# Performance work log

Measured on AMD Instinct MI355X. Metric: run time of the kernel, lower is better.

## Reference

```python
import jax, jax.numpy as jnp
import numpy as np

D_MODEL, N_HEADS = 768, 12
D_K = D_MODEL // N_HEADS
NEG = -1e9


def setup_inputs() -> dict:
    key = jax.random.key(0)
    ks = jax.random.split(key, 12)
    B, S, D = 2, 4096, D_MODEL
    s = 1.0 / np.sqrt(D)
    inp = {
        'query': jax.random.normal(ks[0], (B, S, D), jnp.float32),
        'key': jax.random.normal(ks[1], (B, S, D), jnp.float32),
        'value': jax.random.normal(ks[2], (B, S, D), jnp.float32),
        'mask': jnp.ones((B, S), jnp.int32),
        'Wq': jax.random.normal(ks[3], (D, D), jnp.float32) * s,
        'bq': jnp.zeros((D,), jnp.float32),
        'Wk': jax.random.normal(ks[4], (D, D), jnp.float32) * s,
        'bk': jnp.zeros((D,), jnp.float32),
        'Wv': jax.random.normal(ks[5], (D, D), jnp.float32) * s,
        'bv': jnp.zeros((D,), jnp.float32),
        'Wo': jax.random.normal(ks[6], (D, D), jnp.float32) * s,
        'bo': jnp.zeros((D,), jnp.float32),
    }
    return inp


def reference(query, key, value, mask, Wq, bq, Wk, bk, Wv, bv, Wo, bo):
    B, Sq, D = query.shape
    Sk = key.shape[1]
    # torch Linear: x @ W.T + b; weights stored [out, in]
    def proj(x, W, b, S):
        return (x @ W.T + b).reshape(B, S, N_HEADS, D_K).transpose(0, 2, 1, 3)
    Q = proj(query, Wq, bq, Sq)   # [B,H,Sq,Dk]
    K = proj(key, Wk, bk, Sk)
    V = proj(value, Wv, bv, Sk)
    scores = jnp.einsum('bhqd,bhkd->bhqk', Q, K) / jnp.sqrt(jnp.float32(D_K))
    # padding mask on keys: [B,1,1,Sk]
    scores = jnp.where(mask[:, None, None, :] == 0, NEG, scores)
    # causal mask (triu, diagonal=1)
    causal = jnp.triu(jnp.ones((Sq, Sk), bool), k=1)
    scores = jnp.where(causal[None, None], NEG, scores)
    attn = jax.nn.softmax(scores, axis=-1)
    out = jnp.einsum('bhqk,bhkd->bhqd', attn, V)
    out = out.transpose(0, 2, 1, 3).reshape(B, Sq, D)
    return out @ Wo.T + bo
```

## Files before the change

kernel.cpp:

```cpp
#include <hip/hip_runtime.h>
#include <hip/hip_bf16.h>

#define D_MODEL 768
#define N_HEADS 12
#define D_K     64
#define NEG_INF (-1e9f)
#define SCALE_Q 0.1803368801111154f
#define W_ELEMS (D_MODEL * D_MODEL)

typedef __attribute__((ext_vector_type(8))) short          bf16x8;
typedef __attribute__((ext_vector_type(4))) float          floatx4;
typedef __attribute__((ext_vector_type(4))) unsigned short ushortx4;
typedef __attribute__((ext_vector_type(2))) unsigned int   uintx2;
typedef __attribute__((ext_vector_type(4))) unsigned int   uintx4;

static __device__ __forceinline__ unsigned short f2bf(float f) {
    unsigned u = __builtin_bit_cast(unsigned, f);
    u += 0x7FFFu + ((u >> 16) & 1u);
    return (unsigned short)(u >> 16);
}

static __device__ __forceinline__ float exp2_hw(float x) {
#if __has_builtin(__builtin_amdgcn_exp2f)
    return __builtin_amdgcn_exp2f(x);
#else
    return __builtin_exp2f(x);
#endif
}

static __device__ __forceinline__ float rcp_hw(float x) {
#if __has_builtin(__builtin_amdgcn_rcpf)
    return __builtin_amdgcn_rcpf(x);
#else
    return 1.f / x;
#endif
}

static __device__ __forceinline__ void gload_lds16(const void* g, void* l) {
    __builtin_amdgcn_global_load_lds(
        (const __attribute__((address_space(1))) void*)g,
        (__attribute__((address_space(3))) void*)l, 16, 0, 0);
}

__global__ __launch_bounds__(256) void convert_w4(
    const float* __restrict__ W0, const float* __restrict__ W1,
    const float* __restrict__ W2, const float* __restrict__ W3,
    unsigned short* __restrict__ out)
{
    const float* src[4] = {W0, W1, W2, W3};
    const float* W = src[blockIdx.y];
    unsigned short* o = out + (size_t)blockIdx.y * W_ELEMS;
    const int i = (blockIdx.x * 256 + threadIdx.x) * 4;
    float4 v = *(const float4*)(W + i);
    ushortx4 h = { f2bf(v.x), f2bf(v.y), f2bf(v.z), f2bf(v.w) };
    *(ushortx4*)(o + i) = h;
}

__global__ __launch_bounds__(256) void convert_a3(
    const float* __restrict__ A0, const float* __restrict__ A1,
    const float* __restrict__ A2,
    unsigned short* __restrict__ O0, unsigned short* __restrict__ O1,
    unsigned short* __restrict__ O2)
{
    const int z = blockIdx.y;
    const float* A = (z == 0) ? A0 : (z == 1) ? A1 : A2;
    unsigned short* O = (z == 0) ? O0 : (z == 1) ? O1 : O2;
    const int i = (blockIdx.x * 256 + threadIdx.x) * 4;
    float4 v = *(const float4*)(A + i);
    ushortx4 h = { f2bf(v.x), f2bf(v.y), f2bf(v.z), f2bf(v.w) };
    *(ushortx4*)(O + i) = h;
}

__global__ __launch_bounds__(256) void gemm128(
    const unsigned short* __restrict__ A0, const unsigned short* __restrict__ A1,
    const unsigned short* __restrict__ A2,
    const unsigned short* __restrict__ W0, const unsigned short* __restrict__ W1,
    const unsigned short* __restrict__ W2,
    const float* __restrict__ b0, const float* __restrict__ b1,
    const float* __restrict__ b2,
    void* __restrict__ C0, void* __restrict__ C1, void* __restrict__ C2,
    int S)
{
    __shared__ __align__(16) unsigned short As[128 * 32];
    __shared__ __align__(16) unsigned short Bs[128 * 32];

    const int z = blockIdx.z;
    const unsigned short* A = (z == 0) ? A0 : (z == 1) ? A1 : A2;
    const unsigned short* W = (z == 0) ? W0 : (z == 1) ? W1 : W2;
    const float* bias       = (z == 0) ? b0 : (z == 1) ? b1 : b2;
    void* C                 = (z == 0) ? C0 : (z == 1) ? C1 : C2;
    const float scale = (z == 0) ? SCALE_Q : 1.0f;
    const int mode = (z == 2) ? 3 : 1;

    const int tid  = threadIdx.x;
    const int wave = tid >> 6;
    const int lane = tid & 63;
    const int quad = lane >> 4;
    const int l16  = lane & 15;
    const int m0 = blockIdx.x * 128;
    const int n0 = blockIdx.y * 128;
    const int wm = (wave & 1) * 64;
    const int wn = (wave >> 1) * 64;
    const int sr = lane >> 2;
    const int sc = (lane & 3) << 3;

    const floatx4 zero4 = {0.f, 0.f, 0.f, 0.f};
    floatx4 acc[4][4];
    #pragma unroll
    for (int i = 0; i < 4; ++i)
        #pragma unroll
        for (int j = 0; j < 4; ++j) acc[i][j] = zero4;

    for (int k0 = 0; k0 < D_MODEL; k0 += 32) {
        #pragma unroll
        for (int c = 0; c < 2; ++c) {
            const int row = wave * 32 + c * 16;
            gload_lds16(A + (size_t)(m0 + row + sr) * D_MODEL + k0 + sc,
                        As + row * 32);
            gload_lds16(W + (size_t)(n0 + row + sr) * D_MODEL + k0 + sc,
                        Bs + row * 32);
        }
        __syncthreads();

        bf16x8 af[4], bfr[4];
        #pragma unroll
        for (int i = 0; i < 4; ++i)
            af[i] = *(const bf16x8*)(As + (wm + i * 16 + l16) * 32 + quad * 8);
        #pragma unroll
        for (int j = 0; j < 4; ++j)
            bfr[j] = *(const bf16x8*)(Bs + (wn + j * 16 + l16) * 32 + quad * 8);
        #pragma unroll
        for (int i = 0; i < 4; ++i)
            #pragma unroll
            for (int j = 0; j < 4; ++j)
                acc[i][j] = __builtin_amdgcn_mfma_f32_16x16x32_bf16(
                    bfr[j], af[i], acc[i][j], 0, 0, 0);
        __syncthreads();
    }

    #pragma unroll
    for (int i = 0; i < 4; ++i) {
        const int m = m0 + wm + i * 16 + l16;
        #pragma unroll
        for (int j = 0; j < 4; ++j) {
            const int nb = n0 + wn + j * 16 + quad * 4;
            const float4 bv = *(const float4*)(bias + nb);
            float v0 = (acc[i][j][0] + bv.x) * scale;
            float v1 = (acc[i][j][1] + bv.y) * scale;
            float v2 = (acc[i][j][2] + bv.z) * scale;
            float v3 = (acc[i][j][3] + bv.w) * scale;
            if (mode == 1) {
                ushortx4 o = {f2bf(v0), f2bf(v1), f2bf(v2), f2bf(v3)};
                *(ushortx4*)((unsigned short*)C + (size_t)m * D_MODEL + nb) = o;
            } else {
                const int bb = m / S, s = m - bb * S;
                const int hh = nb >> 6, d = nb & 63;
                unsigned short* base = (unsigned short*)C +
                    ((size_t)(bb * N_HEADS + hh) * D_K + d) * S + s;
                base[0]         = f2bf(v0);
                base[(size_t)S]     = f2bf(v1);
                base[(size_t)S * 2] = f2bf(v2);
                base[(size_t)S * 3] = f2bf(v3);
            }
        }
    }
}

__global__ __launch_bounds__(256) void gemm64o(
    const unsigned short* __restrict__ A,
    const unsigned short* __restrict__ W,
    const float* __restrict__ bias,
    float* __restrict__ C)
{
    __shared__ __align__(16) unsigned short As[64 * 32];
    __shared__ __align__(16) unsigned short Bs[128 * 32];

    const int tid  = threadIdx.x;
    const int wave = tid >> 6;
    const int lane = tid & 63;
    const int quad = lane >> 4;
    const int l16  = lane & 15;
    const int m0 = blockIdx.x * 64;
    const int n0 = blockIdx.y * 128;
    const int wn = wave * 32;
    const int sr = lane >> 2;
    const int sc = (lane & 3) << 3;

    const floatx4 zero4 = {0.f, 0.f, 0.f, 0.f};
    floatx4 acc[4][2];
    #pragma unroll
    for (int i = 0; i < 4; ++i)
        #pragma unroll
        for (int j = 0; j < 2; ++j) acc[i][j] = zero4;

    for (int k0 = 0; k0 < D_MODEL; k0 += 32) {
        if (wave < 2) {
            const int g0 = wave * 32;
            gload_lds16(A + (size_t)(m0 + g0 + sr) * D_MODEL + k0 + sc,
                        As + g0 * 32);
            gload_lds16(A + (size_t)(m0 + g0 + 16 + sr) * D_MODEL + k0 + sc,
                        As + (g0 + 16) * 32);
            const int bg = 96 + wave * 16;
            gload_lds16(W + (size_t)(n0 + bg + sr) * D_MODEL + k0 + sc,
                        Bs + bg * 32);
        } else {
            const int bg = (wave - 2) * 48;
            #pragma unroll
            for (int c = 0; c < 3; ++c)
                gload_lds16(W + (size_t)(n0 + bg + c * 16 + sr) * D_MODEL + k0 + sc,
                            Bs + (bg + c * 16) * 32);
        }
        __syncthreads();

        bf16x8 af[4], bfr[2];
        #pragma unroll
        for (int i = 0; i < 4; ++i)
            af[i] = *(const bf16x8*)(As + (i * 16 + l16) * 32 + quad * 8);
        #pragma unroll
        for (int j = 0; j < 2; ++j)
            bfr[j] = *(const bf16x8*)(Bs + (wn + j * 16 + l16) * 32 + quad * 8);
        #pragma unroll
        for (int i = 0; i < 4; ++i)
            #pragma unroll
            for (int j = 0; j < 2; ++j)
                acc[i][j] = __builtin_amdgcn_mfma_f32_16x16x32_bf16(
                    bfr[j], af[i], acc[i][j], 0, 0, 0);
        __syncthreads();
    }

    #pragma unroll
    for (int i = 0; i < 4; ++i) {
        const int m = m0 + i * 16 + l16;
        #pragma unroll
        for (int j = 0; j < 2; ++j) {
            const int nb = n0 + wn + j * 16 + quad * 4;
            const float4 bv = *(const float4*)(bias + nb);
            float4 o = {acc[i][j][0] + bv.x, acc[i][j][1] + bv.y,
                        acc[i][j][2] + bv.z, acc[i][j][3] + bv.w};
            *(float4*)(C + (size_t)m * D_MODEL + nb) = o;
        }
    }
}

__global__ __launch_bounds__(256) void flash_attn(
    const unsigned short* __restrict__ Qp,
    const unsigned short* __restrict__ Kp,
    const unsigned short* __restrict__ VpT,
    const int* __restrict__ mask,
    unsigned short* __restrict__ O,
    int S)
{
    __shared__ __align__(16) unsigned short Ks [2][64 * 64];
    __shared__ __align__(16) unsigned short Vts[2][64 * 64];
    __shared__ __align__(16) float mskf[2][64];

    const int L  = blockIdx.x;
    const int bh = L % 24;
    const int p  = L / 24;
    const int h  = bh % 12;
    const int b  = bh / 12;
    const int nqt = S >> 6;
    const int tid  = threadIdx.x;
    const int wave = tid >> 6;
    const int lane = tid & 63;
    const int quad = lane >> 4;
    const int l16  = lane & 15;
    const int sx   = (l16 & 7) << 3;
    const int qh   = wave & 1;
    const int kh2  = wave >> 1;

    const unsigned short* Kbase = Kp  + (size_t)(b * S) * D_MODEL + h * D_K;
    const unsigned short* Vbase = VpT + (size_t)(b * N_HEADS + h) * D_K * S;
    const int* mbase = mask + b * S;

    const int srow = wave * 8 + (lane >> 3);
    const int sgc  = ((lane & 7) ^ (lane >> 3)) << 3;

    const floatx4 zero4 = {0.f, 0.f, 0.f, 0.f};
    const short one_bf = (short)0x3F80;
    const bf16x8 ones = {one_bf, one_bf, one_bf, one_bf,
                         one_bf, one_bf, one_bf, one_bf};

    #pragma unroll
    for (int sel = 0; sel < 2; ++sel) {
        const int qt = sel ? (nqt - 1 - p) : p;
        const int q0 = qt * 64;

        bf16x8 qf[2][2];
        #pragma unroll
        for (int qg = 0; qg < 2; ++qg) {
            const size_t rowQ =
                (size_t)(b * S + q0 + qh * 32 + qg * 16 + l16) * D_MODEL + h * D_K;
            qf[qg][0] = *(const bf16x8*)(Qp + rowQ + quad * 8);
            qf[qg][1] = *(const bf16x8*)(Qp + rowQ + 32 + quad * 8);
        }

        floatx4 acc2[2][4];
        floatx4 accl[2];
        #pragma unroll
        for (int qg = 0; qg < 2; ++qg) {
            accl[qg] = zero4;
            #pragma unroll
            for (int dt = 0; dt < 4; ++dt) acc2[qg][dt] = zero4;
        }

        const int ni = qt + 1;

        #pragma unroll
        for (int c = 0; c < 2; ++c) {
            gload_lds16(Kbase + (size_t)(c * 32 + srow) * D_MODEL + sgc,
                        (char*)Ks[0] + (c * 4 + wave) * 1024);
            gload_lds16(Vbase + (size_t)(c * 32 + srow) * S + sgc,
                        (char*)Vts[0] + (c * 4 + wave) * 1024);
        }
        if (tid < 64) mskf[0][tid] = (mbase[tid] == 0) ? NEG_INF : 0.f;
        __syncthreads();

        for (int kt = 0; kt < ni; ++kt) {
            const int k0 = kt * 64;
            const int cur = kt & 1;

            if (kt + 1 < ni) {
                const int kn = k0 + 64;
                #pragma unroll
                for (int c = 0; c < 2; ++c) {
                    gload_lds16(
                        Kbase + (size_t)(kn + c * 32 + srow) * D_MODEL + sgc,
                        (char*)Ks[cur ^ 1] + (c * 4 + wave) * 1024);
                    gload_lds16(
                        Vbase + (size_t)(c * 32 + srow) * S + kn + sgc,
                        (char*)Vts[cur ^ 1] + (c * 4 + wave) * 1024);
                }
                if (tid < 64)
                    mskf[cur ^ 1][tid] = (mbase[kn + tid] == 0) ? NEG_INF : 0.f;
            }

            floatx4 s[2][2];
            __builtin_amdgcn_s_setprio(1);
            #pragma unroll
            for (int nt = 0; nt < 2; ++nt) {
                const int krow = kh2 * 32 + nt * 16 + l16;
                const unsigned short* kro = Ks[cur] + krow * 64;
                const bf16x8 kf0 = *(const bf16x8*)(kro + ((quad * 8) ^ sx));
                const bf16x8 kf1 = *(const bf16x8*)(kro + ((32 + quad * 8) ^ sx));
                const floatx4 cm =
                    *(const floatx4*)(&mskf[cur][kh2 * 32 + nt * 16 + quad * 4]);
                #pragma unroll
                for (int qg = 0; qg < 2; ++qg) {
                    floatx4 c = cm;
                    c = __builtin_amdgcn_mfma_f32_16x16x32_bf16(kf0, qf[qg][0], c, 0, 0, 0);
                    c = __builtin_amdgcn_mfma_f32_16x16x32_bf16(kf1, qf[qg][1], c, 0, 0, 0);
                    s[nt][qg] = c;
                }
            }
            __builtin_amdgcn_s_setprio(0);

            if (kt == ni - 1) {
                #pragma unroll
                for (int nt = 0; nt < 2; ++nt) {
                    const int kb = k0 + kh2 * 32 + nt * 16 + quad * 4;
                    #pragma unroll
                    for (int qg = 0; qg < 2; ++qg) {
                        const int qa = q0 + qh * 32 + qg * 16 + l16;
                        #pragma unroll
                        for (int r = 0; r < 4; ++r)
                            if (kb + r > qa) s[nt][qg][r] = NEG_INF;
                    }
                }
            }

            unsigned pk0[2][2], pk1[2][2];
            #pragma unroll
            for (int nt = 0; nt < 2; ++nt)
                #pragma unroll
                for (int qg = 0; qg < 2; ++qg) {
                    const float e0 = exp2_hw(s[nt][qg][0]);
                    const float e1 = exp2_hw(s[nt][qg][1]);
                    const float e2 = exp2_hw(s[nt][qg][2]);
                    const float e3 = exp2_hw(s[nt][qg][3]);
                    pk0[nt][qg] = __builtin_amdgcn_perm(
                        __builtin_bit_cast(unsigned, e1),
                        __builtin_bit_cast(unsigned, e0), 0x07060302u);
                    pk1[nt][qg] = __builtin_amdgcn_perm(
                        __builtin_bit_cast(unsigned, e3),
                        __builtin_bit_cast(unsigned, e2), 0x07060302u);
                }

            bf16x8 pf[2];
            #pragma unroll
            for (int qg = 0; qg < 2; ++qg) {
                uintx2 a32 = __builtin_amdgcn_permlane32_swap(
                    pk0[0][qg], pk0[1][qg], false, false);
                uintx2 b32 = __builtin_amdgcn_permlane32_swap(
                    pk1[0][qg], pk1[1][qg], false, false);
                uintx2 a16 = __builtin_amdgcn_permlane16_swap(
                    a32[0], a32[1], false, false);
                uintx2 b16 = __builtin_amdgcn_permlane16_swap(
                    b32[0], b32[1], false, false);
                const uintx4 pw = {a16[0], b16[0], a16[1], b16[1]};
                pf[qg] = __builtin_bit_cast(bf16x8, pw);
            }
            __builtin_amdgcn_s_setprio(1);
            #pragma unroll
            for (int dt = 0; dt < 4; ++dt) {
                const int vcol = (kh2 * 32 + quad * 8) ^ sx;
                const bf16x8 vf =
                    *(const bf16x8*)(Vts[cur] + (dt * 16 + l16) * 64 + vcol);
                #pragma unroll
                for (int qg = 0; qg < 2; ++qg)
                    acc2[qg][dt] = __builtin_amdgcn_mfma_f32_16x16x32_bf16(
                        pf[qg], vf, acc2[qg][dt], 0, 0, 0);
            }
            #pragma unroll
            for (int qg = 0; qg < 2; ++qg)
                accl[qg] = __builtin_amdgcn_mfma_f32_16x16x32_bf16(
                    pf[qg], ones, accl[qg], 0, 0, 0);
            __builtin_amdgcn_s_setprio(0);

            __syncthreads();
        }

        float* Kf = (float*)Ks;
        float* Vf = (float*)Vts;
        if (kh2 == 1) {
            #pragma unroll
            for (int qg = 0; qg < 2; ++qg) {
                #pragma unroll
                for (int dt = 0; dt < 4; ++dt)
                    *(floatx4*)(Kf + (qh * 8 + qg * 4 + dt) * 256 + lane * 4) =
                        acc2[qg][dt];
                *(floatx4*)(Vf + (qh * 2 + qg) * 256 + lane * 4) = accl[qg];
            }
        }
        __syncthreads();
        if (kh2 == 0) {
            #pragma unroll
            for (int qg = 0; qg < 2; ++qg) {
                accl[qg] += *(const floatx4*)(Vf + (qh * 2 + qg) * 256 + lane * 4);
                #pragma unroll
                for (int dt = 0; dt < 4; ++dt)
                    acc2[qg][dt] +=
                        *(const floatx4*)(Kf + (qh * 8 + qg * 4 + dt) * 256 + lane * 4);
                #pragma unroll
                for (int r = 0; r < 4; ++r) {
                    const float inv = rcp_hw(accl[qg][r]);
                    const int gq = q0 + qh * 32 + qg * 16 + quad * 4 + r;
                    const size_t base = (size_t)(b * S + gq) * D_MODEL + h * D_K;
                    #pragma unroll
                    for (int dt = 0; dt < 4; ++dt)
                        O[base + dt * 16 + l16] = f2bf(acc2[qg][dt][r] * inv);
                }
            }
        }
        __syncthreads();
    }
}

extern "C" void kernel_launch(void* const* d_in, const int* in_sizes, int n_in,
                              void* d_out, int out_size, void* d_ws, size_t ws_size,
                              hipStream_t stream) {
    const float* query = (const float*)d_in[0];
    const float* key   = (const float*)d_in[1];
    const float* value = (const float*)d_in[2];
    const int*   mask  = (const int*)d_in[3];
    const float* Wq = (const float*)d_in[4];
    const float* bq = (const float*)d_in[5];
    const float* Wk = (const float*)d_in[6];
    const float* bk = (const float*)d_in[7];
    const float* Wv = (const float*)d_in[8];
    const float* bv = (const float*)d_in[9];
    const float* Wo = (const float*)d_in[10];
    const float* bo = (const float*)d_in[11];

    const int B  = 2;
    const int BS = in_sizes[3];
    const int S  = BS / B;
    const int M  = BS;

    unsigned short* Qp  = (unsigned short*)d_ws;
    unsigned short* Kp  = Qp  + (size_t)M * D_MODEL;
    unsigned short* VpT = Kp  + (size_t)M * D_MODEL;
    unsigned short* Obf = VpT + (size_t)M * D_MODEL;
    unsigned short* Wbf = Obf + (size_t)M * D_MODEL;
    unsigned short* Wqb = Wbf;
    unsigned short* Wkb = Wbf + (size_t)W_ELEMS;
    unsigned short* Wvb = Wbf + (size_t)W_ELEMS * 2;
    unsigned short* Wob = Wbf + (size_t)W_ELEMS * 3;
    unsigned short* ka = (unsigned short*)d_out;
    unsigned short* va = ka + (size_t)M * D_MODEL;

    dim3 blk(256);
    convert_w4<<<dim3(W_ELEMS / 1024, 4), blk, 0, stream>>>(Wq, Wk, Wv, Wo, Wbf);
    convert_a3<<<dim3((M * D_MODEL) / 1024, 3), blk, 0, stream>>>(
        query, key, value, Obf, ka, va);

    gemm128<<<dim3(M / 128, D_MODEL / 128, 3), blk, 0, stream>>>(
        Obf, ka, va, Wqb, Wkb, Wvb, bq, bk, bv, Qp, Kp, VpT, S);

    flash_attn<<<768, blk, 0, stream>>>(Qp, Kp, VpT, mask, Obf, S);

    gemm64o<<<dim3(M / 64, D_MODEL / 128), blk, 0, stream>>>(
        Obf, Wob, bo, (float*)d_out);
}
```

Measured before the change: 286.8 us.

## Double-buffer LDS tiles in projection GEMMs to overlap loads with MFMA

Both the QKV projection GEMM and the output projection GEMM now keep two LDS buffers. The next K-slice is issued to the alternate buffer with global-to-LDS loads before the MFMAs on the current slice run. The goal is to hide global load latency behind compute and drop one barrier wait per iteration. In exchange, shared memory per block doubles, which may reduce occupancy. Synchronisation correctness depends on the trailing barrier in the loop body, which is not visible here.

```diff
diff --git a/kernel.cpp b/kernel.cpp
--- a/kernel.cpp
+++ b/kernel.cpp
@@ -81,8 +81,8 @@
     void* __restrict__ C0, void* __restrict__ C1, void* __restrict__ C2,
     int S)
 {
-    __shared__ __align__(16) unsigned short As[128 * 32];
-    __shared__ __align__(16) unsigned short Bs[128 * 32];
+    __shared__ __align__(16) unsigned short As[2][128 * 32];
+    __shared__ __align__(16) unsigned short Bs[2][128 * 32];
 
     const int z = blockIdx.z;
     const unsigned short* A = (z == 0) ? A0 : (z == 1) ? A1 : A2;
@@ -111,24 +111,39 @@
         #pragma unroll
         for (int j = 0; j < 4; ++j) acc[i][j] = zero4;
 
-    for (int k0 = 0; k0 < D_MODEL; k0 += 32) {
-        #pragma unroll
-        for (int c = 0; c < 2; ++c) {
-            const int row = wave * 32 + c * 16;
-            gload_lds16(A + (size_t)(m0 + row + sr) * D_MODEL + k0 + sc,
-                        As + row * 32);
-            gload_lds16(W + (size_t)(n0 + row + sr) * D_MODEL + k0 + sc,
-                        Bs + row * 32);
-        }
-        __syncthreads();
+    #pragma unroll
+    for (int c = 0; c < 2; ++c) {
+        const int row = wave * 32 + c * 16;
+        gload_lds16(A + (size_t)(m0 + row + sr) * D_MODEL + sc,
+                    As[0] + row * 32);
+        gload_lds16(W + (size_t)(n0 + row + sr) * D_MODEL + sc,
+                    Bs[0] + row * 32);
+    }
+    __syncthreads();
+
+    const int NI = D_MODEL / 32;
+    for (int it = 0; it < NI; ++it) {
+        const int cur = it & 1;
+
+        if (it + 1 < NI) {
+            const int kn = (it + 1) * 32;
+            #pragma unroll
+            for (int c = 0; c < 2; ++c) {
+                const int row = wave * 32 + c * 16;
+                gload_lds16(A + (size_t)(m0 + row + sr) * D_MODEL + kn + sc,
+                            As[cur ^ 1] + row * 32);
+                gload_lds16(W + (size_t)(n0 + row + sr) * D_MODEL + kn + sc,
+                            Bs[cur ^ 1] + row * 32);
+            }
+        }
 
         bf16x8 af[4], bfr[4];
         #pragma unroll
         for (int i = 0; i < 4; ++i)
-            af[i] = *(const bf16x8*)(As + (wm + i * 16 + l16) * 32 + quad * 8);
+            af[i] = *(const bf16x8*)(As[cur] + (wm + i * 16 + l16) * 32 + quad * 8);
         #pragma unroll
         for (int j = 0; j < 4; ++j)
-            bfr[j] = *(const bf16x8*)(Bs + (wn + j * 16 + l16) * 32 + quad * 8);
+            bfr[j] = *(const bf16x8*)(Bs[cur] + (wn + j * 16 + l16) * 32 + quad * 8);
         #pragma unroll
         for (int i = 0; i < 4; ++i)
             #pragma unroll
@@ -172,8 +187,8 @@
     const float* __restrict__ bias,
     float* __restrict__ C)
 {
-    __shared__ __align__(16) unsigned short As[64 * 32];
-    __shared__ __align__(16) unsigned short Bs[128 * 32];
+    __shared__ __align__(16) unsigned short As[2][64 * 32];
+    __shared__ __align__(16) unsigned short Bs[2][128 * 32];
 
     const int tid  = threadIdx.x;
     const int wave = tid >> 6;
@@ -193,32 +208,57 @@
         #pragma unroll
         for (int j = 0; j < 2; ++j) acc[i][j] = zero4;
 
-    for (int k0 = 0; k0 < D_MODEL; k0 += 32) {
+    {
         if (wave < 2) {
             const int g0 = wave * 32;
-            gload_lds16(A + (size_t)(m0 + g0 + sr) * D_MODEL + k0 + sc,
-                        As + g0 * 32);
-            gload_lds16(A + (size_t)(m0 + g0 + 16 + sr) * D_MODEL + k0 + sc,
-                        As + (g0 + 16) * 32);
+            gload_lds16(A + (size_t)(m0 + g0 + sr) * D_MODEL + sc,
+                        As[0] + g0 * 32);
+            gload_lds16(A + (size_t)(m0 + g0 + 16 + sr) * D_MODEL + sc,
+                        As[0] + (g0 + 16) * 32);
             const int bg = 96 + wave * 16;
-            gload_lds16(W + (size_t)(n0 + bg + sr) * D_MODEL + k0 + sc,
-                        Bs + bg * 32);
+            gload_lds16(W + (size_t)(n0 + bg + sr) * D_MODEL + sc,
+                        Bs[0] + bg * 32);
         } else {
             const int bg = (wave - 2) * 48;
             #pragma unroll
             for (int c = 0; c < 3; ++c)
-                gload_lds16(W + (size_t)(n0 + bg + c * 16 + sr) * D_MODEL + k0 + sc,
-                            Bs + (bg + c * 16) * 32);
-        }
-        __syncthreads();
+                gload_lds16(W + (size_t)(n0 + bg + c * 16 + sr) * D_MODEL + sc,
+                            Bs[0] + (bg + c * 16) * 32);
+        }
+    }
+    __syncthreads();
+
+    const int NI = D_MODEL / 32;
+    for (int it = 0; it < NI; ++it) {
+        const int cur = it & 1;
+
+        if (it + 1 < NI) {
+            const int kn = (it + 1) * 32;
+            if (wave < 2) {
+                const int g0 = wave * 32;
+                gload_lds16(A + (size_t)(m0 + g0 + sr) * D_MODEL + kn + sc,
+                            As[cur ^ 1] + g0 * 32);
+                gload_lds16(A + (size_t)(m0 + g0 + 16 + sr) * D_MODEL + kn + sc,
+                            As[cur ^ 1] + (g0 + 16) * 32);
+                const int bg = 96 + wave * 16;
+                gload_lds16(W + (size_t)(n0 + bg + sr) * D_MODEL + kn + sc,
+                            Bs[cur ^ 1] + bg * 32);
+            } else {
+                const int bg = (wave - 2) * 48;
+                #pragma unroll
+                for (int c = 0; c < 3; ++c)
+                    gload_lds16(W + (size_t)(n0 + bg + c * 16 + sr) * D_MODEL + kn + sc,
+                                Bs[cur ^ 1] + (bg + c * 16) * 32);
+            }
+        }
 
         bf16x8 af[4], bfr[2];
         #pragma unroll
         for (int i = 0; i < 4; ++i)
-            af[i] = *(const bf16x8*)(As + (i * 16 + l16) * 32 + quad * 8);
+            af[i] = *(const bf16x8*)(As[cur] + (i * 16 + l16) * 32 + quad * 8);
         #pragma unroll
         for (int j = 0; j < 2; ++j)
-            bfr[j] = *(const bf16x8*)(Bs + (wn + j * 16 + l16) * 32 + quad * 8);
+            bfr[j] = *(const bf16x8*)(Bs[cur] + (wn + j * 16 + l16) * 32 + quad * 8);
         #pragma unroll
         for (int i = 0; i < 4; ++i)
             #pragma unroll
```

Result: no change. 285.3 us (-0.5%).
